# Performance work log

Measured on AMD Instinct MI355X. Metric: run time of the kernel, lower is better.

Reference implementation:

```python
import jax, jax.numpy as jnp
import numpy as np

D_IN, D_H, D_OUT = 1024, 1024, 1024
D_MOE = 4096
N_EXPERTS = 8
TOP_K = 2


def setup_inputs() -> dict:
    key = jax.random.key(0)
    ks = jax.random.split(key, 10)
    s = lambda d: 1.0 / np.sqrt(d)
    x = jax.random.normal(ks[0], (2, 2048, D_IN), dtype=jnp.float32)
    W_in = jax.random.normal(ks[1], (D_IN, D_H), dtype=jnp.float32) * s(D_IN)
    b_in = jnp.zeros((D_H,), jnp.float32)
    W_gate = jax.random.normal(ks[2], (D_H, N_EXPERTS), dtype=jnp.float32) * s(D_H)
    b_gate = jnp.zeros((N_EXPERTS,), jnp.float32)
    W1 = jax.random.normal(ks[3], (N_EXPERTS, D_H, D_MOE), dtype=jnp.float32) * s(D_H)
    b1 = jnp.zeros((N_EXPERTS, D_MOE), jnp.float32)
    W2 = jax.random.normal(ks[4], (N_EXPERTS, D_MOE, D_H), dtype=jnp.float32) * s(D_MOE)
    b2 = jnp.zeros((N_EXPERTS, D_H), jnp.float32)
    W_out = jax.random.normal(ks[5], (D_H, D_OUT), dtype=jnp.float32) * s(D_H)
    b_out = jnp.zeros((D_OUT,), jnp.float32)
    return {"x": x, "W_in": W_in, "b_in": b_in, "W_gate": W_gate, "b_gate": b_gate,
            "W1": W1, "b1": b1, "W2": W2, "b2": b2, "W_out": W_out, "b_out": b_out}


def reference(x, W_in, b_in, W_gate, b_gate, W1, b1, W2, b2, W_out, b_out):
    B, S, _ = x.shape
    h = x @ W_in + b_in                       # [B,S,D_H]
    t = h.reshape(B * S, -1)                  # tokens [N,D_H]

    # --- top-k softmax gating ---
    logits = t @ W_gate + b_gate              # [N,E]
    probs = jax.nn.softmax(logits, axis=-1)
    topv, topi = jax.lax.top_k(probs, TOP_K)  # [N,k]
    topv = topv / jnp.sum(topv, axis=-1, keepdims=True)
    # dense routing weights [N,E] (zeros for unselected experts)
    route = jnp.zeros_like(probs).at[jnp.arange(t.shape[0])[:, None], topi].set(topv)

    # --- expert MLPs (dense all-expert compute, weighted combine) ---
    mid = jax.nn.relu(jnp.einsum('nd,edh->neh', t, W1) + b1)   # [N,E,D_MOE]
    eout = jnp.einsum('neh,ehd->ned', mid, W2) + b2            # [N,E,D_H]
    moe_out = jnp.einsum('ne,ned->nd', route, eout)            # [N,D_H]

    out = moe_out.reshape(B, S, -1) @ W_out + b_out            # [B,S,D_OUT]
    return out
```

## Files before the change

kernel.cpp:

```cpp
#include <hip/hip_runtime.h>
#include <hip/hip_bf16.h>

typedef __bf16 bf16_t;
typedef bf16_t bf16x8 __attribute__((ext_vector_type(8)));
typedef bf16_t bf16x4 __attribute__((ext_vector_type(4)));
typedef float f32x4 __attribute__((ext_vector_type(4)));

#define DIN 1024
#define DH 1024
#define DMOE 4096
#define NEXP 8
#define NTOK 4096

__device__ __forceinline__ void gload_lds16(const bf16_t* g, bf16_t* l) {
  __builtin_amdgcn_global_load_lds(
      (const __attribute__((address_space(1))) void*)g,
      (__attribute__((address_space(3))) void*)l, 16, 0, 0);
}

__global__ void k_transpose_all(const float* __restrict__ W_in, const float* __restrict__ W1,
                                const float* __restrict__ W2, const float* __restrict__ W_out,
                                const float* __restrict__ x,
                                bf16_t* __restrict__ WtIn, bf16_t* __restrict__ Wt1,
                                bf16_t* __restrict__ Wt2, bf16_t* __restrict__ WtOut,
                                bf16_t* __restrict__ xbf) {
  const int z = blockIdx.x;
  if (z >= 16896) {
    const int i = (z - 16896) * 256 + threadIdx.x;
    const float4 v = *(const float4*)(x + (size_t)i * 4);
    bf16x4 o;
    o.x = (bf16_t)v.x; o.y = (bf16_t)v.y; o.z = (bf16_t)v.z; o.w = (bf16_t)v.w;
    *(bf16x4*)(xbf + (size_t)i * 4) = o;
    return;
  }
  const float* s; bf16_t* d; int R, C, tx, ty;
  if (z < 256) {
    s = W_in; d = WtIn; R = DIN; C = DH; tx = z & 15; ty = z >> 4;
  } else if (z < 8448) {
    const int l = z - 256, e = l >> 10, t = l & 1023;
    s = W1 + (size_t)e * DH * DMOE; d = Wt1 + (size_t)e * DH * DMOE;
    R = DH; C = DMOE; tx = t & 63; ty = t >> 6;
  } else if (z < 16640) {
    const int l = z - 8448, e = l >> 10, t = l & 1023;
    s = W2 + (size_t)e * DMOE * DH; d = Wt2 + (size_t)e * DMOE * DH;
    R = DMOE; C = DH; tx = t & 15; ty = t >> 4;
  } else {
    const int t = z - 16640;
    s = W_out; d = WtOut; R = DH; C = DH; tx = t & 15; ty = t >> 4;
  }
  __shared__ float tile[64][65];
  const int c0 = tx * 64, r0 = ty * 64;
  const int t = threadIdx.x;
  const int rr = t >> 4;
  const int cc = (t & 15) << 2;
#pragma unroll
  for (int i = 0; i < 64; i += 16) {
    const float4 v = *(const float4*)&s[(size_t)(r0 + rr + i) * C + c0 + cc];
    tile[rr + i][cc + 0] = v.x;
    tile[rr + i][cc + 1] = v.y;
    tile[rr + i][cc + 2] = v.z;
    tile[rr + i][cc + 3] = v.w;
  }
  __syncthreads();
  const int orr = (t & 7) * 8;
  const int oc = t >> 3;
#pragma unroll
  for (int i = 0; i < 64; i += 32) {
    bf16x8 o;
#pragma unroll
    for (int j = 0; j < 8; ++j) o[j] = (bf16_t)tile[orr + j][oc + i];
    *(bf16x8*)&d[(size_t)(c0 + oc + i) * R + r0 + orr] = o;
  }
}

__global__ void k_gate_prep(const float* __restrict__ Win, const float* __restrict__ Wgate,
                            const float* __restrict__ b_in, const float* __restrict__ b_gate,
                            double* __restrict__ G, double* __restrict__ cvec,
                            int* __restrict__ cnt) {
  if (blockIdx.x == 0 && threadIdx.x < 8) cnt[threadIdx.x] = 0;
  const int lane = threadIdx.x & 63;
  const int wave = (blockIdx.x * blockDim.x + threadIdx.x) >> 6;
  const int nw = (gridDim.x * blockDim.x) >> 6;
  for (int d = wave; d <= DIN; d += nw) {
    const float* row = (d < DIN) ? (Win + (size_t)d * DH) : b_in;
    double acc[8] = {0, 0, 0, 0, 0, 0, 0, 0};
    for (int k = lane; k < DH; k += 64) {
      const double xv = (double)row[k];
      const float* g = Wgate + (size_t)k * NEXP;
#pragma unroll
      for (int ee = 0; ee < 8; ++ee) acc[ee] += xv * (double)g[ee];
    }
#pragma unroll
    for (int ee = 0; ee < 8; ++ee) {
      double a = acc[ee];
      for (int o = 32; o > 0; o >>= 1) a += __shfl_down(a, o);
      acc[ee] = a;
    }
    if (lane == 0) {
      if (d < DIN) {
#pragma unroll
        for (int ee = 0; ee < 8; ++ee) G[(size_t)d * 8 + ee] = acc[ee];
      } else {
#pragma unroll
        for (int ee = 0; ee < 8; ++ee) cvec[ee] = acc[ee] + (double)b_gate[ee];
      }
    }
  }
}

__global__ void k_gating(const float* __restrict__ x, const double* __restrict__ G,
                         const double* __restrict__ cvec, int* __restrict__ cnt,
                         int* __restrict__ list, float* __restrict__ wlist) {
  const int lane = threadIdx.x & 63;
  const int t = blockIdx.x * (blockDim.x >> 6) + (threadIdx.x >> 6);
  if (t >= NTOK) return;
  const float* xr = x + (size_t)t * DIN;
  double acc[8] = {0, 0, 0, 0, 0, 0, 0, 0};
  for (int d = lane; d < DIN; d += 64) {
    const double xv = (double)xr[d];
    const double* g = G + (size_t)d * 8;
#pragma unroll
    for (int ee = 0; ee < 8; ++ee) acc[ee] += xv * g[ee];
  }
#pragma unroll
  for (int ee = 0; ee < 8; ++ee) {
    double a = acc[ee];
    for (int o = 32; o > 0; o >>= 1) a += __shfl_down(a, o);
    acc[ee] = a;
  }
  if (lane == 0) {
    double l[8];
#pragma unroll
    for (int ee = 0; ee < 8; ++ee) l[ee] = acc[ee] + cvec[ee];
    double m = l[0];
#pragma unroll
    for (int ee = 1; ee < 8; ++ee) m = fmax(m, l[ee]);
    double p[8];
#pragma unroll
    for (int ee = 0; ee < 8; ++ee) p[ee] = exp(l[ee] - m);
    int i1 = 0;
#pragma unroll
    for (int ee = 1; ee < 8; ++ee)
      if (p[ee] > p[i1]) i1 = ee;
    int i2 = (i1 == 0) ? 1 : 0;
#pragma unroll
    for (int ee = 0; ee < 8; ++ee)
      if (ee != i1 && p[ee] > p[i2]) i2 = ee;
    const double s2 = p[i1] + p[i2];
    const float w1 = (float)(p[i1] / s2);
    const float w2 = (float)(p[i2] / s2);
    int lp = atomicAdd(&cnt[i1], 1);
    list[i1 * NTOK + lp] = t * 2;
    wlist[i1 * NTOK + lp] = w1;
    lp = atomicAdd(&cnt[i2], 1);
    list[i2 * NTOK + lp] = t * 2 + 1;
    wlist[i2 * NTOK + lp] = w2;
  }
}

__global__ void k_scan(const int* __restrict__ cnt, int* __restrict__ offs) {
  if (threadIdx.x == 0) {
    int s = 0;
    for (int e = 0; e < NEXP; ++e) { offs[e] = s; s += cnt[e]; }
    offs[NEXP] = s;
  }
}

__global__ void k_combine4(const bf16_t* __restrict__ ebf, bf16_t* __restrict__ moebf) {
  const int i = blockIdx.x * blockDim.x + threadIdx.x;
  const int t = i >> 8;
  const int q = (i & 255) * 4;
  const bf16x4 a = *(const bf16x4*)(ebf + ((size_t)t * 2) * DH + q);
  const bf16x4 b = *(const bf16x4*)(ebf + ((size_t)t * 2 + 1) * DH + q);
  const bf16x4 c = *(const bf16x4*)(ebf + ((size_t)(2 * NTOK + t * 2)) * DH + q);
  const bf16x4 d = *(const bf16x4*)(ebf + ((size_t)(2 * NTOK + t * 2 + 1)) * DH + q);
  bf16x4 o;
  o.x = (bf16_t)((float)a.x + (float)b.x + (float)c.x + (float)d.x);
  o.y = (bf16_t)((float)a.y + (float)b.y + (float)c.y + (float)d.y);
  o.z = (bf16_t)((float)a.z + (float)b.z + (float)c.z + (float)d.z);
  o.w = (bf16_t)((float)a.w + (float)b.w + (float)c.w + (float)d.w);
  *(bf16x4*)(moebf + (size_t)t * DH + q) = o;
}

template <int OUT_F32>
__global__ __launch_bounds__(256, 3) void k_gemm_plain(
    const bf16_t* __restrict__ A, const bf16_t* __restrict__ B,
    const float* __restrict__ bias, void* __restrict__ Cbase,
    int M, int N, int K) {
  const int mblk = blockIdx.y, nblk = blockIdx.x;

  __shared__ bf16_t As[3][128 * 32];
  __shared__ bf16_t Bs[3][128 * 32];

  const int tid = threadIdx.x;
  const int lane = tid & 63;
  const int wid = tid >> 6;
  const int wr = wid >> 1, wc = wid & 1;

  const int srow0 = wid * 32 + (lane >> 2);
  const int srow1 = srow0 + 16;
  const int skcol = ((lane & 3) ^ ((lane >> 3) & 3)) * 8;

  const bf16_t* aptr0 = A + (size_t)(mblk * 128 + srow0) * K + skcol;
  const bf16_t* aptr1 = A + (size_t)(mblk * 128 + srow1) * K + skcol;
  const bf16_t* bptr0 = B + (size_t)(nblk * 128 + srow0) * K + skcol;
  const bf16_t* bptr1 = B + (size_t)(nblk * 128 + srow1) * K + skcol;

  const int ldsOfsA0 = (wid * 32) * 32;
  const int ldsOfsA1 = (wid * 32 + 16) * 32;

  f32x4 acc[4][4] = {};
  const int nkt = K >> 5;

  auto stage = [&](int buf, int kt) {
    const size_t ko = (size_t)kt * 32;
    gload_lds16(aptr0 + ko, &As[buf][ldsOfsA0]);
    gload_lds16(aptr1 + ko, &As[buf][ldsOfsA1]);
    gload_lds16(bptr0 + ko, &Bs[buf][ldsOfsA0]);
    gload_lds16(bptr1 + ko, &Bs[buf][ldsOfsA1]);
  };

  stage(0, 0);
  if (nkt > 1) stage(1, 1);

  const int fr = lane & 15;
  const int s0 = (((lane >> 4) ^ ((fr >> 1) & 3)) << 3);

  int cur = 0;
  for (int kt = 0; kt < nkt; ++kt) {
    int nxt = cur + 2;
    if (nxt >= 3) nxt -= 3;
    if (kt + 2 < nkt) {
      stage(nxt, kt + 2);
      asm volatile("s_waitcnt vmcnt(8)" ::: "memory");
    } else if (kt + 1 < nkt) {
      asm volatile("s_waitcnt vmcnt(4)" ::: "memory");
    } else {
      asm volatile("s_waitcnt vmcnt(0)" ::: "memory");
    }
    __builtin_amdgcn_s_barrier();

    bf16x8 af[4], bfr[4];
#pragma unroll
    for (int m = 0; m < 4; ++m)
      af[m] = *(const bf16x8*)&As[cur][(wr * 64 + m * 16 + fr) * 32 + s0];
#pragma unroll
    for (int n = 0; n < 4; ++n)
      bfr[n] = *(const bf16x8*)&Bs[cur][(wc * 64 + n * 16 + fr) * 32 + s0];
#pragma unroll
    for (int m = 0; m < 4; ++m)
#pragma unroll
      for (int n = 0; n < 4; ++n)
        acc[m][n] = __builtin_amdgcn_mfma_f32_16x16x32_bf16(af[m], bfr[n], acc[m][n], 0, 0, 0);

    __builtin_amdgcn_s_barrier();
    cur += 1;
    if (cur >= 3) cur -= 3;
  }

  const int colBase = nblk * 128 + wc * 64 + (lane & 15);
  const int rowBase = mblk * 128 + wr * 64 + ((lane >> 4) << 2);
#pragma unroll
  for (int n = 0; n < 4; ++n) {
    const int c = colBase + n * 16;
    const float bv = bias[c];
#pragma unroll
    for (int m = 0; m < 4; ++m) {
#pragma unroll
      for (int j = 0; j < 4; ++j) {
        const int r = rowBase + m * 16 + j;
        const float v = acc[m][n][j] + bv;
        if constexpr (OUT_F32 == 0) {
          ((bf16_t*)Cbase)[(size_t)r * N + c] = (bf16_t)v;
        } else {
          ((float*)Cbase)[(size_t)r * N + c] = v;
        }
      }
    }
  }
}

__global__ __launch_bounds__(512, 4) void k_gemm1(
    const bf16_t* __restrict__ Abase, const bf16_t* __restrict__ Bbase,
    const float* __restrict__ biasBase, bf16_t* __restrict__ Cbase,
    int N, int K,
    const int* __restrict__ cnt, const int* __restrict__ offs,
    const int* __restrict__ listBase) {
  const int e = blockIdx.z;
  const int mblk = blockIdx.y, nblk = blockIdx.x;
  const int Mloc = cnt[e];
  if (mblk * 256 >= Mloc) return;
  const bf16_t* B = Bbase + (size_t)e * N * K;
  const float* bias = biasBase + (size_t)e * N;
  const int* myList = listBase + e * NTOK;
  const int rowOff = offs[e];

  __shared__ bf16_t As[3][256 * 32];
  __shared__ bf16_t Bs[3][128 * 32];

  const int tid = threadIdx.x;
  const int lane = tid & 63;
  const int wid = tid >> 6;
  const int wr = wid >> 1, wc = wid & 1;

  const int subr = lane >> 2;
  const int skcol = ((lane & 3) ^ ((lane >> 3) & 3)) * 8;

  uint32_t aofs[2];
#pragma unroll
  for (int l = 0; l < 2; ++l) {
    int ar = mblk * 256 + (wid * 2 + l) * 16 + subr;
    if (ar > Mloc - 1) ar = Mloc - 1;
    aofs[l] = (uint32_t)(myList[ar] >> 1) * (uint32_t)K + skcol;
  }
  const uint32_t bofs = (uint32_t)(nblk * 128 + wid * 16 + subr) * (uint32_t)K + skcol;

  f32x4 acc[4][4] = {};
  const int nkt = K >> 5;

  auto stage = [&](int buf, int kt) {
    const uint32_t ko = (uint32_t)kt * 32;
    gload_lds16(Abase + aofs[0] + ko, &As[buf][(wid * 2 + 0) * 512]);
    gload_lds16(Abase + aofs[1] + ko, &As[buf][(wid * 2 + 1) * 512]);
    gload_lds16(B + bofs + ko, &Bs[buf][wid * 512]);
  };

  stage(0, 0);
  if (nkt > 1) stage(1, 1);

  const int fr = lane & 15;
  const int s0 = (((lane >> 4) ^ ((fr >> 1) & 3)) << 3);

  int cur = 0;
  for (int kt = 0; kt < nkt; ++kt) {
    int nxt = cur + 2;
    if (nxt >= 3) nxt -= 3;
    if (kt + 2 < nkt) {
      stage(nxt, kt + 2);
      asm volatile("s_waitcnt vmcnt(6)" ::: "memory");
    } else if (kt + 1 < nkt) {
      asm volatile("s_waitcnt vmcnt(3)" ::: "memory");
    } else {
      asm volatile("s_waitcnt vmcnt(0)" ::: "memory");
    }
    __builtin_amdgcn_s_barrier();

    bf16x8 af[4], bfr[4];
#pragma unroll
    for (int m = 0; m < 4; ++m)
      af[m] = *(const bf16x8*)&As[cur][(wr * 64 + m * 16 + fr) * 32 + s0];
#pragma unroll
    for (int n = 0; n < 4; ++n)
      bfr[n] = *(const bf16x8*)&Bs[cur][(wc * 64 + n * 16 + fr) * 32 + s0];
#pragma unroll
    for (int m = 0; m < 4; ++m)
#pragma unroll
      for (int n = 0; n < 4; ++n)
        acc[m][n] = __builtin_amdgcn_mfma_f32_16x16x32_bf16(af[m], bfr[n], acc[m][n], 0, 0, 0);

    __builtin_amdgcn_s_barrier();
    cur += 1;
    if (cur >= 3) cur -= 3;
  }

  const int colBase = nblk * 128 + wc * 64 + (lane & 15);
  const int rowBase = mblk * 256 + wr * 64 + ((lane >> 4) << 2);
#pragma unroll
  for (int n = 0; n < 4; ++n) {
    const int c = colBase + n * 16;
    const float bv = bias[c];
#pragma unroll
    for (int m = 0; m < 4; ++m) {
#pragma unroll
      for (int j = 0; j < 4; ++j) {
        const int r = rowBase + m * 16 + j;
        if (r < Mloc) {
          Cbase[(size_t)(rowOff + r) * N + c] = (bf16_t)fmaxf(acc[m][n][j] + bv, 0.0f);
        }
      }
    }
  }
}

__global__ __launch_bounds__(256, 3) void k_gemm2s(
    const bf16_t* __restrict__ Abase, const bf16_t* __restrict__ Bbase,
    const float* __restrict__ biasBase, bf16_t* __restrict__ Cbase,
    int N, int K,
    const int* __restrict__ cnt, const int* __restrict__ offs,
    const int* __restrict__ listBase, const float* __restrict__ wlistBase) {
  const int e = blockIdx.z >> 1;
  const int half = blockIdx.z & 1;
  const int mblk = blockIdx.y, nblk = blockIdx.x;
  const int Mloc = cnt[e];
  if (mblk * 128 >= Mloc) return;
  const bf16_t* B = Bbase + (size_t)e * N * K;
  const float* bias = biasBase + (size_t)e * N;
  const int* myList = listBase + e * NTOK;
  const float* myW = wlistBase + e * NTOK;
  const bf16_t* A = Abase + (size_t)offs[e] * K;
  const uint32_t kbase = (uint32_t)half * (uint32_t)(K >> 1);

  __shared__ bf16_t As[3][128 * 32];
  __shared__ bf16_t Bs[3][128 * 32];

  const int tid = threadIdx.x;
  const int lane = tid & 63;
  const int wid = tid >> 6;
  const int wr = wid >> 1, wc = wid & 1;

  const int srow0 = wid * 32 + (lane >> 2);
  const int srow1 = srow0 + 16;
  const int skcol = ((lane & 3) ^ ((lane >> 3) & 3)) * 8;

  int ar0 = mblk * 128 + srow0;
  int ar1 = mblk * 128 + srow1;
  if (ar0 > Mloc - 1) ar0 = Mloc - 1;
  if (ar1 > Mloc - 1) ar1 = Mloc - 1;
  const bf16_t* aptr0 = A + (size_t)ar0 * K + kbase + skcol;
  const bf16_t* aptr1 = A + (size_t)ar1 * K + kbase + skcol;
  const bf16_t* bptr0 = B + (size_t)(nblk * 128 + srow0) * K + kbase + skcol;
  const bf16_t* bptr1 = B + (size_t)(nblk * 128 + srow1) * K + kbase + skcol;

  const int ldsOfsA0 = (wid * 32) * 32;
  const int ldsOfsA1 = (wid * 32 + 16) * 32;

  f32x4 acc[4][4] = {};
  const int nkt = K >> 6;

  auto stage = [&](int buf, int kt) {
    const size_t ko = (size_t)kt * 32;
    gload_lds16(aptr0 + ko, &As[buf][ldsOfsA0]);
    gload_lds16(aptr1 + ko, &As[buf][ldsOfsA1]);
    gload_lds16(bptr0 + ko, &Bs[buf][ldsOfsA0]);
    gload_lds16(bptr1 + ko, &Bs[buf][ldsOfsA1]);
  };

  stage(0, 0);
  if (nkt > 1) stage(1, 1);

  const int fr = lane & 15;
  const int s0 = (((lane >> 4) ^ ((fr >> 1) & 3)) << 3);

  int cur = 0;
  for (int kt = 0; kt < nkt; ++kt) {
    int nxt = cur + 2;
    if (nxt >= 3) nxt -= 3;
    if (kt + 2 < nkt) {
      stage(nxt, kt + 2);
      asm volatile("s_waitcnt vmcnt(8)" ::: "memory");
    } else if (kt + 1 < nkt) {
      asm volatile("s_waitcnt vmcnt(4)" ::: "memory");
    } else {
      asm volatile("s_waitcnt vmcnt(0)" ::: "memory");
    }
    __builtin_amdgcn_s_barrier();

    bf16x8 af[4], bfr[4];
#pragma unroll
    for (int m = 0; m < 4; ++m)
      af[m] = *(const bf16x8*)&As[cur][(wr * 64 + m * 16 + fr) * 32 + s0];
#pragma unroll
    for (int n = 0; n < 4; ++n)
      bfr[n] = *(const bf16x8*)&Bs[cur][(wc * 64 + n * 16 + fr) * 32 + s0];
#pragma unroll
    for (int m = 0; m < 4; ++m)
#pragma unroll
      for (int n = 0; n < 4; ++n)
        acc[m][n] = __builtin_amdgcn_mfma_f32_16x16x32_bf16(af[m], bfr[n], acc[m][n], 0, 0, 0);

    __builtin_amdgcn_s_barrier();
    cur += 1;
    if (cur >= 3) cur -= 3;
  }

  const int colBase = nblk * 128 + wc * 64 + (lane & 15);
  const int rowBase = mblk * 128 + wr * 64 + ((lane >> 4) << 2);
  const size_t outOfs = (size_t)half * 2 * NTOK * DH;
#pragma unroll
  for (int n = 0; n < 4; ++n) {
    const int c = colBase + n * 16;
    const float bv = half ? 0.0f : bias[c];
#pragma unroll
    for (int m = 0; m < 4; ++m) {
#pragma unroll
      for (int j = 0; j < 4; ++j) {
        const int r = rowBase + m * 16 + j;
        if (r < Mloc) {
          const int entry = myList[r];
          const float w = myW[r];
          Cbase[outOfs + (size_t)entry * DH + c] = (bf16_t)((acc[m][n][j] + bv) * w);
        }
      }
    }
  }
}


extern "C" void kernel_launch(void* const* d_in, const int* in_sizes, int n_in,
                              void* d_out, int out_size, void* d_ws, size_t ws_size,
                              hipStream_t stream) {
  const float* x      = (const float*)d_in[0];
  const float* W_in   = (const float*)d_in[1];
  const float* b_in   = (const float*)d_in[2];
  const float* W_gate = (const float*)d_in[3];
  const float* b_gate = (const float*)d_in[4];
  const float* W1     = (const float*)d_in[5];
  const float* b1     = (const float*)d_in[6];
  const float* W2     = (const float*)d_in[7];
  const float* b2     = (const float*)d_in[8];
  const float* W_out  = (const float*)d_in[9];
  const float* b_out  = (const float*)d_in[10];

  char* ws = (char*)d_ws;
  size_t off = 0;
  auto alloc = [&](size_t bytes) -> void* {
    void* p = ws + off;
    off += (bytes + 255) & ~(size_t)255;
    return p;
  };

  bf16_t* WtIn  = (bf16_t*)alloc((size_t)DH * DIN * 2);
  bf16_t* Wt1   = (bf16_t*)alloc((size_t)NEXP * DMOE * DH * 2);
  bf16_t* Wt2   = (bf16_t*)alloc((size_t)NEXP * DH * DMOE * 2);
  bf16_t* WtOut = (bf16_t*)alloc((size_t)DH * DH * 2);
  bf16_t* xbf   = (bf16_t*)alloc((size_t)NTOK * DIN * 2);
  bf16_t* hbf   = (bf16_t*)alloc((size_t)NTOK * DH * 2);
  bf16_t* mid   = (bf16_t*)alloc((size_t)2 * NTOK * DMOE * 2);
  bf16_t* ebf   = (bf16_t*)alloc((size_t)2 * 2 * NTOK * DH * 2);
  bf16_t* moebf = (bf16_t*)alloc((size_t)NTOK * DH * 2);
  double* G     = (double*)alloc((size_t)DIN * 8 * 8);
  double* cvec  = (double*)alloc(8 * 8);
  int*    cnt   = (int*)alloc(NEXP * 4);
  int*    offs  = (int*)alloc((NEXP + 1) * 4);
  int*    list  = (int*)alloc((size_t)NEXP * NTOK * 4);
  float*  wlist = (float*)alloc((size_t)NEXP * NTOK * 4);

  k_transpose_all<<<20992, 256, 0, stream>>>(W_in, W1, W2, W_out, x,
                                             WtIn, Wt1, Wt2, WtOut, xbf);

  k_gate_prep<<<64, 256, 0, stream>>>(W_in, W_gate, b_in, b_gate, G, cvec, cnt);
  k_gating<<<NTOK / 4, 256, 0, stream>>>(x, G, cvec, cnt, list, wlist);
  k_scan<<<1, 64, 0, stream>>>(cnt, offs);

  k_gemm_plain<0><<<dim3(DH / 128, NTOK / 128, 1), 256, 0, stream>>>(
      xbf, WtIn, b_in, hbf, NTOK, DH, DIN);
  k_gemm1<<<dim3(DMOE / 128, NTOK / 256, NEXP), 512, 0, stream>>>(
      hbf, Wt1, b1, mid, DMOE, DH, cnt, offs, list);
  k_gemm2s<<<dim3(DH / 128, NTOK / 128, NEXP * 2), 256, 0, stream>>>(
      mid, Wt2, b2, ebf, DH, DMOE, cnt, offs, list, wlist);
  k_combine4<<<NTOK * DH / 4 / 256, 256, 0, stream>>>(ebf, moebf);
  k_gemm_plain<1><<<dim3(DH / 128, NTOK / 128, 1), 256, 0, stream>>>(
      moebf, WtOut, b_out, (float*)d_out, NTOK, DH, DH);
}
```

Measured before the change: 568.9 us.

## Drop split-K in expert GEMM2 and compute expert row offsets in-kernel

Expert GEMM2 no longer splits K into two halves across the z grid. Each block now runs the full K=4096 reduction and writes one partial per token-expert slot, so the combine kernel reads two inputs instead of four. The separate scan kernel is removed and each GEMM block sums the preceding expert counts itself. This cuts one launch and half the combine traffic and intermediate memory, but halves the number of GEMM2 blocks, which may leave CUs underused given the per-expert row imbalance.

```diff
diff --git a/kernel.cpp b/kernel.cpp
--- a/kernel.cpp
+++ b/kernel.cpp
@@ -158,27 +158,17 @@
   }
 }
 
-__global__ void k_scan(const int* __restrict__ cnt, int* __restrict__ offs) {
-  if (threadIdx.x == 0) {
-    int s = 0;
-    for (int e = 0; e < NEXP; ++e) { offs[e] = s; s += cnt[e]; }
-    offs[NEXP] = s;
-  }
-}
-
-__global__ void k_combine4(const bf16_t* __restrict__ ebf, bf16_t* __restrict__ moebf) {
+__global__ void k_combine(const bf16_t* __restrict__ eout, bf16_t* __restrict__ moebf) {
   const int i = blockIdx.x * blockDim.x + threadIdx.x;
   const int t = i >> 8;
   const int q = (i & 255) * 4;
-  const bf16x4 a = *(const bf16x4*)(ebf + ((size_t)t * 2) * DH + q);
-  const bf16x4 b = *(const bf16x4*)(ebf + ((size_t)t * 2 + 1) * DH + q);
-  const bf16x4 c = *(const bf16x4*)(ebf + ((size_t)(2 * NTOK + t * 2)) * DH + q);
-  const bf16x4 d = *(const bf16x4*)(ebf + ((size_t)(2 * NTOK + t * 2 + 1)) * DH + q);
+  const bf16x4 a = *(const bf16x4*)(eout + ((size_t)t * 2) * DH + q);
+  const bf16x4 b = *(const bf16x4*)(eout + ((size_t)t * 2 + 1) * DH + q);
   bf16x4 o;
-  o.x = (bf16_t)((float)a.x + (float)b.x + (float)c.x + (float)d.x);
-  o.y = (bf16_t)((float)a.y + (float)b.y + (float)c.y + (float)d.y);
-  o.z = (bf16_t)((float)a.z + (float)b.z + (float)c.z + (float)d.z);
-  o.w = (bf16_t)((float)a.w + (float)b.w + (float)c.w + (float)d.w);
+  o.x = (bf16_t)((float)a.x + (float)b.x);
+  o.y = (bf16_t)((float)a.y + (float)b.y);
+  o.z = (bf16_t)((float)a.z + (float)b.z);
+  o.w = (bf16_t)((float)a.w + (float)b.w);
   *(bf16x4*)(moebf + (size_t)t * DH + q) = o;
 }
 
@@ -284,16 +274,16 @@
     const bf16_t* __restrict__ Abase, const bf16_t* __restrict__ Bbase,
     const float* __restrict__ biasBase, bf16_t* __restrict__ Cbase,
     int N, int K,
-    const int* __restrict__ cnt, const int* __restrict__ offs,
-    const int* __restrict__ listBase) {
+    const int* __restrict__ cnt, const int* __restrict__ listBase) {
   const int e = blockIdx.z;
   const int mblk = blockIdx.y, nblk = blockIdx.x;
   const int Mloc = cnt[e];
   if (mblk * 256 >= Mloc) return;
+  int rowOff = 0;
+  for (int i = 0; i < NEXP; ++i) rowOff += (i < e) ? cnt[i] : 0;
   const bf16_t* B = Bbase + (size_t)e * N * K;
   const float* bias = biasBase + (size_t)e * N;
   const int* myList = listBase + e * NTOK;
-  const int rowOff = offs[e];
 
   __shared__ bf16_t As[3][256 * 32];
   __shared__ bf16_t Bs[3][128 * 32];
@@ -382,23 +372,23 @@
   }
 }
 
-__global__ __launch_bounds__(256, 3) void k_gemm2s(
+__global__ __launch_bounds__(256, 3) void k_gemm_e2(
     const bf16_t* __restrict__ Abase, const bf16_t* __restrict__ Bbase,
     const float* __restrict__ biasBase, bf16_t* __restrict__ Cbase,
     int N, int K,
-    const int* __restrict__ cnt, const int* __restrict__ offs,
-    const int* __restrict__ listBase, const float* __restrict__ wlistBase) {
-  const int e = blockIdx.z >> 1;
-  const int half = blockIdx.z & 1;
+    const int* __restrict__ cnt, const int* __restrict__ listBase,
+    const float* __restrict__ wlistBase) {
+  const int e = blockIdx.z;
   const int mblk = blockIdx.y, nblk = blockIdx.x;
   const int Mloc = cnt[e];
   if (mblk * 128 >= Mloc) return;
+  int rowOff = 0;
+  for (int i = 0; i < NEXP; ++i) rowOff += (i < e) ? cnt[i] : 0;
   const bf16_t* B = Bbase + (size_t)e * N * K;
   const float* bias = biasBase + (size_t)e * N;
   const int* myList = listBase + e * NTOK;
   const float* myW = wlistBase + e * NTOK;
-  const bf16_t* A = Abase + (size_t)offs[e] * K;
-  const uint32_t kbase = (uint32_t)half * (uint32_t)(K >> 1);
+  const bf16_t* A = Abase + (size_t)rowOff * K;
 
   __shared__ bf16_t As[3][128 * 32];
   __shared__ bf16_t Bs[3][128 * 32];
@@ -416,16 +406,16 @@
   int ar1 = mblk * 128 + srow1;
   if (ar0 > Mloc - 1) ar0 = Mloc - 1;
   if (ar1 > Mloc - 1) ar1 = Mloc - 1;
-  const bf16_t* aptr0 = A + (size_t)ar0 * K + kbase + skcol;
-  const bf16_t* aptr1 = A + (size_t)ar1 * K + kbase + skcol;
-  const bf16_t* bptr0 = B + (size_t)(nblk * 128 + srow0) * K + kbase + skcol;
-  const bf16_t* bptr1 = B + (size_t)(nblk * 128 + srow1) * K + kbase + skcol;
+  const bf16_t* aptr0 = A + (size_t)ar0 * K + skcol;
+  const bf16_t* aptr1 = A + (size_t)ar1 * K + skcol;
+  const bf16_t* bptr0 = B + (size_t)(nblk * 128 + srow0) * K + skcol;
+  const bf16_t* bptr1 = B + (size_t)(nblk * 128 + srow1) * K + skcol;
 
   const int ldsOfsA0 = (wid * 32) * 32;
   const int ldsOfsA1 = (wid * 32 + 16) * 32;
 
   f32x4 acc[4][4] = {};
-  const int nkt = K >> 6;
+  const int nkt = K >> 5;
 
   auto stage = [&](int buf, int kt) {
     const size_t ko = (size_t)kt * 32;
@@ -475,11 +465,10 @@
 
   const int colBase = nblk * 128 + wc * 64 + (lane & 15);
   const int rowBase = mblk * 128 + wr * 64 + ((lane >> 4) << 2);
-  const size_t outOfs = (size_t)half * 2 * NTOK * DH;
 #pragma unroll
   for (int n = 0; n < 4; ++n) {
     const int c = colBase + n * 16;
-    const float bv = half ? 0.0f : bias[c];
+    const float bv = bias[c];
 #pragma unroll
     for (int m = 0; m < 4; ++m) {
 #pragma unroll
@@ -488,7 +477,7 @@
         if (r < Mloc) {
           const int entry = myList[r];
           const float w = myW[r];
-          Cbase[outOfs + (size_t)entry * DH + c] = (bf16_t)((acc[m][n][j] + bv) * w);
+          Cbase[(size_t)entry * DH + c] = (bf16_t)((acc[m][n][j] + bv) * w);
         }
       }
     }
@@ -526,12 +515,11 @@
   bf16_t* xbf   = (bf16_t*)alloc((size_t)NTOK * DIN * 2);
   bf16_t* hbf   = (bf16_t*)alloc((size_t)NTOK * DH * 2);
   bf16_t* mid   = (bf16_t*)alloc((size_t)2 * NTOK * DMOE * 2);
-  bf16_t* ebf   = (bf16_t*)alloc((size_t)2 * 2 * NTOK * DH * 2);
+  bf16_t* eoutb = (bf16_t*)alloc((size_t)2 * NTOK * DH * 2);
   bf16_t* moebf = (bf16_t*)alloc((size_t)NTOK * DH * 2);
   double* G     = (double*)alloc((size_t)DIN * 8 * 8);
   double* cvec  = (double*)alloc(8 * 8);
   int*    cnt   = (int*)alloc(NEXP * 4);
-  int*    offs  = (int*)alloc((NEXP + 1) * 4);
   int*    list  = (int*)alloc((size_t)NEXP * NTOK * 4);
   float*  wlist = (float*)alloc((size_t)NEXP * NTOK * 4);
 
@@ -540,15 +528,14 @@
 
   k_gate_prep<<<64, 256, 0, stream>>>(W_in, W_gate, b_in, b_gate, G, cvec, cnt);
   k_gating<<<NTOK / 4, 256, 0, stream>>>(x, G, cvec, cnt, list, wlist);
-  k_scan<<<1, 64, 0, stream>>>(cnt, offs);
 
   k_gemm_plain<0><<<dim3(DH / 128, NTOK / 128, 1), 256, 0, stream>>>(
       xbf, WtIn, b_in, hbf, NTOK, DH, DIN);
   k_gemm1<<<dim3(DMOE / 128, NTOK / 256, NEXP), 512, 0, stream>>>(
-      hbf, Wt1, b1, mid, DMOE, DH, cnt, offs, list);
-  k_gemm2s<<<dim3(DH / 128, NTOK / 128, NEXP * 2), 256, 0, stream>>>(
-      mid, Wt2, b2, ebf, DH, DMOE, cnt, offs, list, wlist);
-  k_combine4<<<NTOK * DH / 4 / 256, 256, 0, stream>>>(ebf, moebf);
+      hbf, Wt1, b1, mid, DMOE, DH, cnt, list);
+  k_gemm_e2<<<dim3(DH / 128, NTOK / 128, NEXP), 256, 0, stream>>>(
+      mid, Wt2, b2, eoutb, DH, DMOE, cnt, list, wlist);
+  k_combine<<<NTOK * DH / 4 / 256, 256, 0, stream>>>(eoutb, moebf);
   k_gemm_plain<1><<<dim3(DH / 128, NTOK / 128, 1), 256, 0, stream>>>(
       moebf, WtOut, b_out, (float*)d_out, NTOK, DH, DH);
 }
```

New measurement: 556.5 us. 1.02x faster.
